# Optimization experiments

Hardware: AMD Instinct MI355X
Metric: run time of the kernel (lower is better)

The kernel has to match this reference:

```python
import jax, jax.numpy as jnp
import numpy as np
import math

D_MODEL = 256
N_LEVELS = 4
N_HEADS = 8
N_POINTS = 4
N_FRAME = 4
SHAPES = [(80, 80), (40, 40), (20, 20), (10, 10)]  # sum H*W = 8500
NB = 2
T1 = 4
T2 = 4
LEN_Q = 8500


def _grid_init_bias():
    # replicate torch _reset_parameters grid bias for sampling_offsets
    thetas = np.arange(N_HEADS, dtype=np.float32) * (2.0 * math.pi / N_HEADS)
    grid = np.stack([np.cos(thetas), np.sin(thetas)], -1)
    grid = grid / np.abs(grid).max(-1, keepdims=True)
    grid = np.tile(grid[:, None, None, :], (1, N_LEVELS, N_POINTS, 1))
    grid = grid * (np.arange(N_POINTS, dtype=np.float32) + 1.0)[None, None, :, None]
    return jnp.asarray(grid.reshape(-1), jnp.float32)


def setup_inputs() -> dict:
    key = jax.random.key(0)
    ks = jax.random.split(key, 8)
    Len_in = sum(h * w for h, w in SHAPES)
    query = jax.random.normal(ks[0], (NB, T1, LEN_Q, D_MODEL), jnp.float32)
    reference_points = jax.random.uniform(ks[1], (NB, T1, LEN_Q, N_LEVELS, 2), jnp.float32)
    input_flatten = jax.random.normal(ks[2], (NB, T2, Len_in, D_MODEL), jnp.float32)
    input_spatial_shapes = jnp.array(SHAPES, jnp.int32)
    starts = np.cumsum([0] + [h * w for h, w in SHAPES])[:-1]
    input_level_start_index = jnp.asarray(starts, jnp.int32)
    s = 0.01
    W_off = jax.random.normal(ks[3], (D_MODEL, N_HEADS * N_LEVELS * N_POINTS * 2), jnp.float32) * s
    b_off = _grid_init_bias()
    W_att = jax.random.normal(ks[4], (D_MODEL, N_HEADS * N_LEVELS * N_POINTS), jnp.float32) * s
    b_att = jnp.zeros((N_HEADS * N_LEVELS * N_POINTS,), jnp.float32)
    xav = 1.0 / math.sqrt(D_MODEL)
    W_val = jax.random.normal(ks[5], (D_MODEL, D_MODEL), jnp.float32) * xav
    b_val = jnp.zeros((D_MODEL,), jnp.float32)
    W_out = jax.random.normal(ks[6], (D_MODEL, D_MODEL), jnp.float32) * xav
    b_out = jnp.zeros((D_MODEL,), jnp.float32)
    return dict(query=query, reference_points=reference_points, input_flatten=input_flatten,
                input_spatial_shapes=input_spatial_shapes, input_level_start_index=input_level_start_index,
                W_off=W_off, b_off=b_off, W_att=W_att, b_att=b_att,
                W_val=W_val, b_val=b_val, W_out=W_out, b_out=b_out)


def _bilinear(v_flat, H, W, gx, gy):
    # v_flat: (B, d, H*W); gx,gy: (B, S) in [-1,1]; zeros padding, align_corners=False
    x = (gx + 1.0) * (W * 0.5) - 0.5
    y = (gy + 1.0) * (H * 0.5) - 0.5
    x0 = jnp.floor(x); y0 = jnp.floor(y)
    x1 = x0 + 1.0; y1 = y0 + 1.0
    wx1 = x - x0; wx0 = 1.0 - wx1
    wy1 = y - y0; wy0 = 1.0 - wy1

    def gather(xi, yi):
        valid = ((xi >= 0) & (xi < W) & (yi >= 0) & (yi < H)).astype(v_flat.dtype)
        xc = jnp.clip(xi, 0, W - 1).astype(jnp.int32)
        yc = jnp.clip(yi, 0, H - 1).astype(jnp.int32)
        idx = yc * W + xc  # (B, S)
        g = jnp.take_along_axis(v_flat, idx[:, None, :], axis=2)  # (B, d, S)
        return g * valid[:, None, :]

    return (gather(x0, y0) * (wx0 * wy0)[:, None, :]
            + gather(x1, y0) * (wx1 * wy0)[:, None, :]
            + gather(x0, y1) * (wx0 * wy1)[:, None, :]
            + gather(x1, y1) * (wx1 * wy1)[:, None, :])


def _core(value_t, locs, att, shapes):
    # value_t: (n, Len_in, M, d); locs: (n, Lq, M, L, P, 2); att: (n, Lq, M, L, P)
    n, Len_in, M, d = value_t.shape
    Lq, P = locs.shape[1], locs.shape[4]
    start = 0
    out = 0.0
    for l, (H, W) in enumerate(shapes):
        hw = H * W
        v = value_t[:, start:start + hw]  # (n, hw, M, d)
        start += hw
        v = v.transpose(0, 2, 3, 1).reshape(n * M, d, hw)
        g = locs[:, :, :, l] * 2.0 - 1.0  # (n, Lq, M, P, 2)
        g = g.transpose(0, 2, 1, 3, 4).reshape(n * M, Lq * P, 2)
        samp = _bilinear(v, H, W, g[..., 0], g[..., 1])  # (n*M, d, Lq*P)
        a = att[:, :, :, l].transpose(0, 2, 1, 3).reshape(n * M, 1, Lq * P)
        out = out + (samp * a).reshape(n, M, d, Lq, P).sum(-1)
    return out.transpose(0, 3, 1, 2).reshape(n, Lq, M * d)  # (n, Lq, C)


def reference(query, reference_points, input_flatten, input_spatial_shapes, input_level_start_index,
              W_off, b_off, W_att, b_att, W_val, b_val, W_out, b_out):
    shapes = [(int(h), int(w)) for h, w in np.asarray(input_spatial_shapes)]
    n, t1n, Lq, C = query.shape
    M, L, P = N_HEADS, N_LEVELS, N_POINTS
    d = C // M
    value = input_flatten @ W_val + b_val  # (n, T2, Len_in, C)
    value = value.reshape(n, value.shape[1], -1, M, d)
    normalizer = jnp.array([[w, h] for h, w in shapes], jnp.float32)  # (L, 2) = (W_l, H_l)
    outs = []
    for t1 in range(t1n):
        t2s = [t for t in (t1 - 1, t1, t1 + 1) if 0 <= t < N_FRAME]
        K = len(t2s)
        q = query[:, t1]  # (n, Lq, C)
        # all frames share ONE attention_weights Linear -> identical logits per t2
        logits = (q @ W_att + b_att).reshape(n, Lq, M, L, P)
        stacked = jnp.broadcast_to(logits[..., None], (n, Lq, M, L, P, K))
        att = jax.nn.softmax(stacked.reshape(n, Lq, M, L * P * K), axis=-1)
        att = att.reshape(n, Lq, M, L, P, K)
        # all frames share ONE sampling_offsets Linear -> identical locations per t2
        off = (q @ W_off + b_off).reshape(n, Lq, M, L, P, 2)
        off = off / normalizer[None, None, None, :, None, :]
        locs = reference_points[:, t1][:, :, None, :, None, :] + off  # (n,Lq,M,L,P,2)
        out_t1 = 0.0
        for k, t2 in enumerate(t2s):
            out_t1 = out_t1 + _core(value[:, t2], locs, att[..., k], shapes)
        outs.append(out_t1)
    out = jnp.stack(outs, axis=1)  # (n, T1, Lq, C)
    return out @ W_out + b_out
```

## Files before the change

### kernel.cpp

```cpp
#include <hip/hip_runtime.h>

#define LQ 8500

typedef _Float16 half8 __attribute__((ext_vector_type(8)));
typedef float f32x4 __attribute__((ext_vector_type(4)));

__device__ __forceinline__ unsigned short f2h(float f) {
    return __builtin_bit_cast(unsigned short, (_Float16)f);
}
__device__ __forceinline__ float hlo(unsigned w) {
    return (float)__builtin_bit_cast(_Float16, (unsigned short)(w & 0xffffu));
}
__device__ __forceinline__ float hhi(unsigned w) {
    return (float)__builtin_bit_cast(_Float16, (unsigned short)(w >> 16));
}
__device__ __forceinline__ unsigned pk2(float a, float b) {
    return (unsigned)f2h(a) | ((unsigned)f2h(b) << 16);
}

__global__ __launch_bounds__(256) void prep_weights(const float* __restrict__ Woff,
                                                    const float* __restrict__ boff,
                                                    const float* __restrict__ Watt,
                                                    const float* __restrict__ batt,
                                                    const float* __restrict__ Wval,
                                                    const float* __restrict__ Wout,
                                                    unsigned short* __restrict__ Wct,
                                                    unsigned short* __restrict__ Wvt,
                                                    unsigned short* __restrict__ Wot,
                                                    float* __restrict__ bcat) {
    int idx = blockIdx.x * 256 + threadIdx.x;
    if (idx < 98304) {
        int j = idx >> 8, k = idx & 255;
        float v = (j < 256) ? Woff[k * 256 + j] : Watt[k * 128 + (j - 256)];
        Wct[idx] = f2h(v);
    } else if (idx < 98304 + 65536) {
        int t = idx - 98304;
        int n = t >> 8, k = t & 255;
        Wvt[t] = f2h(Wval[k * 256 + n]);
    } else if (idx < 98304 + 131072) {
        int t = idx - 98304 - 65536;
        int n = t >> 8, k = t & 255;
        Wot[t] = f2h(Wout[k * 256 + n]);
    } else if (idx < 98304 + 131072 + 384) {
        int j = idx - 98304 - 131072;
        bcat[j] = (j < 256) ? boff[j] : batt[j - 256];
    }
}

template <int OUTMODE, int ASRC>
__global__ __launch_bounds__(256) void gemm_f16(const void* __restrict__ Avoid,
                                                const unsigned short* __restrict__ Bt,
                                                const float* __restrict__ bias,
                                                void* __restrict__ Cout, int M) {
    __shared__ char lds[32768];
    const int tid = threadIdx.x;
    const int r0 = blockIdx.x * 128, c0 = blockIdx.y * 128;
    const int wid = tid >> 6, lane = tid & 63;
    const int wr = (wid >> 1) * 64, wc = (wid & 1) * 64;

    f32x4 acc[4][4] = {};
    uint4 ra[2], rb[2];

#define LOADT(k0)                                                                      \
    {                                                                                  \
        _Pragma("unroll")                                                              \
        for (int cc = 0; cc < 2; ++cc) {                                               \
            int ch = cc * 256 + tid;                                                   \
            int row = ch >> 2, seg = ch & 3;                                           \
            uint4 va = {0, 0, 0, 0};                                                   \
            int ar = r0 + row;                                                         \
            if (ar < M) {                                                              \
                if (ASRC == 0) {                                                       \
                    va = *reinterpret_cast<const uint4*>(                              \
                        (const unsigned short*)Avoid + (size_t)ar * 256 + (k0) + seg * 8); \
                } else {                                                               \
                    const float4* ap = reinterpret_cast<const float4*>(                \
                        (const float*)Avoid + (size_t)ar * 256 + (k0) + seg * 8);      \
                    float4 a = ap[0], b = ap[1];                                       \
                    va.x = pk2(a.x, a.y); va.y = pk2(a.z, a.w);                        \
                    va.z = pk2(b.x, b.y); va.w = pk2(b.z, b.w);                        \
                }                                                                      \
            }                                                                          \
            ra[cc] = va;                                                               \
            rb[cc] = *reinterpret_cast<const uint4*>(Bt + (size_t)(c0 + row) * 256 +   \
                                                     (k0) + seg * 8);                  \
        }                                                                              \
    }

#define STORET(b)                                                                      \
    {                                                                                  \
        _Pragma("unroll")                                                              \
        for (int cc = 0; cc < 2; ++cc) {                                               \
            int ch = cc * 256 + tid;                                                   \
            int row = ch >> 2, seg = ch & 3;                                           \
            int byte = (row << 6) + (seg << 4);                                        \
            int swz = byte ^ ((row & 7) << 4);                                         \
            *reinterpret_cast<uint4*>(lds + (b) * 16384 + swz) = ra[cc];               \
            *reinterpret_cast<uint4*>(lds + (b) * 16384 + 8192 + swz) = rb[cc];        \
        }                                                                              \
    }

    LOADT(0);
    STORET(0);
    __syncthreads();

    for (int t = 0; t < 8; ++t) {
        if (t < 7) LOADT((t + 1) * 32);
        char* base = lds + (t & 1) * 16384;
        half8 af[4], bf[4];
#pragma unroll
        for (int i = 0; i < 4; ++i) {
            int rowA = wr + i * 16 + (lane & 15);
            int byteA = (rowA << 6) + ((lane >> 4) << 4);
            af[i] = *reinterpret_cast<const half8*>(base + (byteA ^ ((rowA & 7) << 4)));
            int rowB = wc + i * 16 + (lane & 15);
            int byteB = (rowB << 6) + ((lane >> 4) << 4);
            bf[i] = *reinterpret_cast<const half8*>(base + 8192 + (byteB ^ ((rowB & 7) << 4)));
        }
#pragma unroll
        for (int i = 0; i < 4; ++i)
#pragma unroll
            for (int j = 0; j < 4; ++j)
                acc[i][j] = __builtin_amdgcn_mfma_f32_16x16x32_f16(af[i], bf[j], acc[i][j], 0, 0, 0);
        if (t < 7) STORET((t + 1) & 1);
        __syncthreads();
    }

#pragma unroll
    for (int j = 0; j < 4; ++j) {
        int col = c0 + wc + j * 16 + (lane & 15);
        float bv = (OUTMODE == 3) ? 0.f : bias[col];
#pragma unroll
        for (int i = 0; i < 4; ++i) {
#pragma unroll
            for (int r = 0; r < 4; ++r) {
                int row = r0 + wr + i * 16 + (lane >> 4) * 4 + r;
                if (row >= M) continue;
                float v = acc[i][j][r];
                if (OUTMODE == 2) {
                    ((unsigned short*)Cout)[(size_t)row * 384 + col] = f2h(v + bv);
                } else if (OUTMODE == 3) {
                    ((unsigned short*)Cout)[(size_t)row * 256 + col] = f2h(v);
                } else {
                    ((float*)Cout)[(size_t)row * 256 + col] = v + bv;
                }
            }
        }
    }
#undef LOADT
#undef STORET
}

__global__ __launch_bounds__(256) void vsum_kernel(const unsigned short* __restrict__ Y,
                                                   const float* __restrict__ bval,
                                                   unsigned short* __restrict__ Vs) {
    int plane = blockIdx.y;
    int g = plane >> 3, m = plane & 7;
    int t1 = g & 3, n = g >> 2;
    int f = blockIdx.x * 256 + threadIdx.x;
    if (f >= LQ * 4) return;
    int pos = f >> 2, c8 = (f & 3) * 8;
    float Kc = (t1 == 0 || t1 == 3) ? 2.f : 3.f;
    const float* bp = bval + m * 32 + c8;
    float acc[8];
#pragma unroll
    for (int j = 0; j < 8; ++j) acc[j] = Kc * bp[j];
    int t2a = t1 == 0 ? 0 : t1 - 1;
    int t2b = t1 == 3 ? 3 : t1 + 1;
    for (int t2 = t2a; t2 <= t2b; ++t2) {
        uint4 v = *reinterpret_cast<const uint4*>(
            Y + ((size_t)(n * 4 + t2) * LQ + pos) * 256 + m * 32 + c8);
        acc[0] += hlo(v.x); acc[1] += hhi(v.x);
        acc[2] += hlo(v.y); acc[3] += hhi(v.y);
        acc[4] += hlo(v.z); acc[5] += hhi(v.z);
        acc[6] += hlo(v.w); acc[7] += hhi(v.w);
    }
    uint4 o;
    o.x = pk2(acc[0], acc[1]); o.y = pk2(acc[2], acc[3]);
    o.z = pk2(acc[4], acc[5]); o.w = pk2(acc[6], acc[7]);
    *reinterpret_cast<uint4*>(Vs + ((size_t)plane * LQ + pos) * 32 + c8) = o;
}

__global__ __launch_bounds__(256) void sample_kernel(const unsigned short* __restrict__ P,
                                                     const float* __restrict__ refp,
                                                     const unsigned short* __restrict__ Vs,
                                                     unsigned short* __restrict__ O16) {
    int tid = threadIdx.x, bid = blockIdx.x;
    int g = bid & 7;
    int q0 = (bid >> 3) * 16;
    int ql = tid >> 4, m = (tid >> 1) & 7, h = tid & 1;
    int q = q0 + ql;
    if (q >= LQ) return;

    const size_t qrow = (size_t)g * LQ + q;

    unsigned ow[16];
    {
        const uint4* po = reinterpret_cast<const uint4*>(P + qrow * 384 + m * 32);
        uint4 a = po[0], b = po[1], c = po[2], d = po[3];
        ow[0] = a.x; ow[1] = a.y; ow[2] = a.z; ow[3] = a.w;
        ow[4] = b.x; ow[5] = b.y; ow[6] = b.z; ow[7] = b.w;
        ow[8] = c.x; ow[9] = c.y; ow[10] = c.z; ow[11] = c.w;
        ow[12] = d.x; ow[13] = d.y; ow[14] = d.z; ow[15] = d.w;
    }
    float wgt[16];
    {
        const uint4* pa = reinterpret_cast<const uint4*>(P + qrow * 384 + 256 + m * 16);
        uint4 a = pa[0], b = pa[1];
        unsigned aw[8] = {a.x, a.y, a.z, a.w, b.x, b.y, b.z, b.w};
#pragma unroll
        for (int j = 0; j < 8; ++j) {
            wgt[j * 2 + 0] = hlo(aw[j]);
            wgt[j * 2 + 1] = hhi(aw[j]);
        }
        float mx = -1e30f;
#pragma unroll
        for (int j = 0; j < 16; ++j) mx = fmaxf(mx, wgt[j]);
        float s = 0.f;
#pragma unroll
        for (int j = 0; j < 16; ++j) { wgt[j] = __expf(wgt[j] - mx); s += wgt[j]; }
        int t1 = g & 3;
        float Kc = (t1 == 0 || t1 == 3) ? 2.f : 3.f;
        float inv = 1.f / (s * Kc);
#pragma unroll
        for (int j = 0; j < 16; ++j) wgt[j] *= inv;
    }

    float rx[4], ry[4];
    {
        const float4* rp = reinterpret_cast<const float4*>(refp + qrow * 8);
        float4 r0 = rp[0], r1 = rp[1];
        rx[0] = r0.x; ry[0] = r0.y; rx[1] = r0.z; ry[1] = r0.w;
        rx[2] = r1.x; ry[2] = r1.y; rx[3] = r1.z; ry[3] = r1.w;
    }

    float acc[16];
#pragma unroll
    for (int d = 0; d < 16; ++d) acc[d] = 0.f;

    const unsigned short* vplane = Vs + (size_t)(g * 8 + m) * (LQ * 32) + h * 16;

#pragma unroll 4
    for (int p = 0; p < 16; ++p) {
        const int l = p >> 2;
        const int Wl = 80 >> l;
        const int start = (l == 0) ? 0 : (l == 1) ? 6400 : (l == 2) ? 8000 : 8400;
        const float Wlf = (float)Wl;

        float x = fmaf(rx[l], Wlf, hlo(ow[p])) - 0.5f;
        float y = fmaf(ry[l], Wlf, hhi(ow[p])) - 0.5f;
        float w = wgt[p];

        float xf = floorf(x), yf = floorf(y);
        int x0 = (int)xf, y0 = (int)yf;
        float wx1 = x - xf, wy1 = y - yf;

        int xb = min(max(x0, 0), Wl - 2);
        float wl = (x0 == xb) ? 1.f - wx1 : ((x0 + 1 == xb) ? wx1 : 0.f);
        float wr = (x0 == xb) ? wx1 : ((x0 - 1 == xb) ? 1.f - wx1 : 0.f);

        int yc0 = min(max(y0, 0), Wl - 1);
        float cw0 = (y0 >= 0 && y0 < Wl) ? (1.f - wy1) * w : 0.f;
        int y1i = y0 + 1;
        int yc1 = min(max(y1i, 0), Wl - 1);
        float cw1 = (y1i >= 0 && y1i < Wl) ? wy1 * w : 0.f;

        const uint4* p0 = reinterpret_cast<const uint4*>(
            vplane + (size_t)(start + yc0 * Wl + xb) * 32);
        const uint4* p1 = reinterpret_cast<const uint4*>(
            vplane + (size_t)(start + yc1 * Wl + xb) * 32);
        uint4 L0a = p0[0], L0b = p0[1], R0a = p0[4], R0b = p0[5];
        uint4 L1a = p1[0], L1b = p1[1], R1a = p1[4], R1b = p1[5];

        float c0l = cw0 * wl, c0r = cw0 * wr;
        float c1l = cw1 * wl, c1r = cw1 * wr;

        acc[0]  += c0l * hlo(L0a.x) + c0r * hlo(R0a.x) + c1l * hlo(L1a.x) + c1r * hlo(R1a.x);
        acc[1]  += c0l * hhi(L0a.x) + c0r * hhi(R0a.x) + c1l * hhi(L1a.x) + c1r * hhi(R1a.x);
        acc[2]  += c0l * hlo(L0a.y) + c0r * hlo(R0a.y) + c1l * hlo(L1a.y) + c1r * hlo(R1a.y);
        acc[3]  += c0l * hhi(L0a.y) + c0r * hhi(R0a.y) + c1l * hhi(L1a.y) + c1r * hhi(R1a.y);
        acc[4]  += c0l * hlo(L0a.z) + c0r * hlo(R0a.z) + c1l * hlo(L1a.z) + c1r * hlo(R1a.z);
        acc[5]  += c0l * hhi(L0a.z) + c0r * hhi(R0a.z) + c1l * hhi(L1a.z) + c1r * hhi(R1a.z);
        acc[6]  += c0l * hlo(L0a.w) + c0r * hlo(R0a.w) + c1l * hlo(L1a.w) + c1r * hlo(R1a.w);
        acc[7]  += c0l * hhi(L0a.w) + c0r * hhi(R0a.w) + c1l * hhi(L1a.w) + c1r * hhi(R1a.w);
        acc[8]  += c0l * hlo(L0b.x) + c0r * hlo(R0b.x) + c1l * hlo(L1b.x) + c1r * hlo(R1b.x);
        acc[9]  += c0l * hhi(L0b.x) + c0r * hhi(R0b.x) + c1l * hhi(L1b.x) + c1r * hhi(R1b.x);
        acc[10] += c0l * hlo(L0b.y) + c0r * hlo(R0b.y) + c1l * hlo(L1b.y) + c1r * hlo(R1b.y);
        acc[11] += c0l * hhi(L0b.y) + c0r * hhi(R0b.y) + c1l * hhi(L1b.y) + c1r * hhi(R1b.y);
        acc[12] += c0l * hlo(L0b.z) + c0r * hlo(R0b.z) + c1l * hlo(L1b.z) + c1r * hlo(R1b.z);
        acc[13] += c0l * hhi(L0b.z) + c0r * hhi(R0b.z) + c1l * hhi(L1b.z) + c1r * hhi(R1b.z);
        acc[14] += c0l * hlo(L0b.w) + c0r * hlo(R0b.w) + c1l * hlo(L1b.w) + c1r * hlo(R1b.w);
        acc[15] += c0l * hhi(L0b.w) + c0r * hhi(R0b.w) + c1l * hhi(L1b.w) + c1r * hhi(R1b.w);
    }

    unsigned short* op = O16 + qrow * 256 + m * 32 + h * 16;
    uint4 o0, o1;
    o0.x = pk2(acc[0], acc[1]);   o0.y = pk2(acc[2], acc[3]);
    o0.z = pk2(acc[4], acc[5]);   o0.w = pk2(acc[6], acc[7]);
    o1.x = pk2(acc[8], acc[9]);   o1.y = pk2(acc[10], acc[11]);
    o1.z = pk2(acc[12], acc[13]); o1.w = pk2(acc[14], acc[15]);
    reinterpret_cast<uint4*>(op)[0] = o0;
    reinterpret_cast<uint4*>(op)[1] = o1;
}

extern "C" void kernel_launch(void* const* d_in, const int* in_sizes, int n_in,
                              void* d_out, int out_size, void* d_ws, size_t ws_size,
                              hipStream_t stream) {
    const float* query = (const float*)d_in[0];
    const float* refp  = (const float*)d_in[1];
    const float* inp   = (const float*)d_in[2];
    const float* Woff = (const float*)d_in[5];
    const float* boff = (const float*)d_in[6];
    const float* Watt = (const float*)d_in[7];
    const float* batt = (const float*)d_in[8];
    const float* Wval = (const float*)d_in[9];
    const float* bval = (const float*)d_in[10];
    const float* Wout = (const float*)d_in[11];
    const float* bout = (const float*)d_in[12];
    float* out = (float*)d_out;

    char* base = (char*)d_ws;
    unsigned short* Y    = (unsigned short*)base;
    unsigned short* O16  = (unsigned short*)base;
    unsigned short* Vs   = (unsigned short*)(base + 34816000);
    unsigned short* P    = (unsigned short*)(base + 69632000);
    unsigned short* Wct  = (unsigned short*)(base + 121856000);
    unsigned short* Wvt  = (unsigned short*)(base + 122052608);
    unsigned short* Wot  = (unsigned short*)(base + 122183680);
    float* bcat          = (float*)(base + 122314752);

    const int RT = (8 * LQ + 127) / 128;

    prep_weights<<<dim3(898), 256, 0, stream>>>(Woff, boff, Watt, batt, Wval, Wout,
                                                Wct, Wvt, Wot, bcat);

    gemm_f16<3, 1><<<dim3(RT, 2), 256, 0, stream>>>(inp, Wvt, bcat, Y, 8 * LQ);

    vsum_kernel<<<dim3((LQ * 4 + 255) / 256, 64), 256, 0, stream>>>(Y, bval, Vs);

    gemm_f16<2, 1><<<dim3(RT, 3), 256, 0, stream>>>(query, Wct, bcat, P, 8 * LQ);

    sample_kernel<<<dim3(((LQ + 15) / 16) * 8), 256, 0, stream>>>(P, refp, Vs, O16);

    gemm_f16<0, 0><<<dim3(RT, 2), 256, 0, stream>>>(O16, Wot, bout, out, 8 * LQ);
}
```

Measured before the change: 331.1 us.

## Merge value and query projection GEMMs and stage operands via direct global-to-LDS loads

The value projection and the query offset/attention projection are now issued as one launch with five column-block groups, so the two independent GEMMs share a grid and one launch is removed. Operand tiles that are already fp16 (weights, and both operands of the output GEMM) are copied straight into LDS with global_load_lds instead of passing through registers. An inverse-swizzle mapping keeps the existing bank-conflict-free LDS layout. The risk is correctness of the inverse swizzle against the per-wave LDS base layout, and that the output GEMM skips A rows past M, which leaves stale LDS data for those rows.

```diff
diff --git a/kernel.cpp b/kernel.cpp
--- a/kernel.cpp
+++ b/kernel.cpp
@@ -16,6 +16,12 @@
 }
 __device__ __forceinline__ unsigned pk2(float a, float b) {
     return (unsigned)f2h(a) | ((unsigned)f2h(b) << 16);
+}
+
+__device__ __forceinline__ void gl_lds16(const unsigned short* gsrc, char* ldst) {
+    __builtin_amdgcn_global_load_lds(
+        (const __attribute__((address_space(1))) void*)gsrc,
+        (__attribute__((address_space(3))) void*)ldst, 16, 0, 0);
 }
 
 __global__ __launch_bounds__(256) void prep_weights(const float* __restrict__ Woff,
@@ -47,67 +53,94 @@
     }
 }
 
-template <int OUTMODE, int ASRC>
-__global__ __launch_bounds__(256) void gemm_f16(const void* __restrict__ Avoid,
-                                                const unsigned short* __restrict__ Bt,
-                                                const float* __restrict__ bias,
-                                                void* __restrict__ Cout, int M) {
+__device__ __forceinline__ void inv_swz(int d, int& brow, int& bseg) {
+    int b8 = (d >> 8) & 1;
+    int rm = (((d >> 6) & 1) ^ b8) | (((d >> 7) & 1) << 1) | (b8 << 2);
+    int b = d ^ (rm << 4);
+    brow = b >> 6;
+    bseg = (b >> 4) & 3;
+}
+
+__global__ __launch_bounds__(256) void gemm_yp(const float* __restrict__ inp,
+                                               const float* __restrict__ query,
+                                               const unsigned short* __restrict__ Wvt,
+                                               const unsigned short* __restrict__ Wct,
+                                               const float* __restrict__ bcat,
+                                               unsigned short* __restrict__ Yo,
+                                               unsigned short* __restrict__ Po) {
     __shared__ char lds[32768];
     const int tid = threadIdx.x;
-    const int r0 = blockIdx.x * 128, c0 = blockIdx.y * 128;
+    const int r0 = blockIdx.x * 128;
+    const int yb = blockIdx.y;
+    const bool isY = yb < 2;
+    const int c0 = isY ? yb * 128 : (yb - 2) * 128;
+    const float* A = isY ? inp : query;
+    const unsigned short* Bt = isY ? Wvt : Wct;
     const int wid = tid >> 6, lane = tid & 63;
     const int wr = (wid >> 1) * 64, wc = (wid & 1) * 64;
+    const int M = 8 * LQ;
+
+    int browc[2], bsegc[2];
+#pragma unroll
+    for (int cc = 0; cc < 2; ++cc)
+        inv_swz((cc * 256 + tid) << 4, browc[cc], bsegc[cc]);
 
     f32x4 acc[4][4] = {};
-    uint4 ra[2], rb[2];
-
-#define LOADT(k0)                                                                      \
-    {                                                                                  \
-        _Pragma("unroll")                                                              \
-        for (int cc = 0; cc < 2; ++cc) {                                               \
-            int ch = cc * 256 + tid;                                                   \
-            int row = ch >> 2, seg = ch & 3;                                           \
-            uint4 va = {0, 0, 0, 0};                                                   \
-            int ar = r0 + row;                                                         \
-            if (ar < M) {                                                              \
-                if (ASRC == 0) {                                                       \
-                    va = *reinterpret_cast<const uint4*>(                              \
-                        (const unsigned short*)Avoid + (size_t)ar * 256 + (k0) + seg * 8); \
-                } else {                                                               \
-                    const float4* ap = reinterpret_cast<const float4*>(                \
-                        (const float*)Avoid + (size_t)ar * 256 + (k0) + seg * 8);      \
-                    float4 a = ap[0], b = ap[1];                                       \
-                    va.x = pk2(a.x, a.y); va.y = pk2(a.z, a.w);                        \
-                    va.z = pk2(b.x, b.y); va.w = pk2(b.z, b.w);                        \
-                }                                                                      \
-            }                                                                          \
-            ra[cc] = va;                                                               \
-            rb[cc] = *reinterpret_cast<const uint4*>(Bt + (size_t)(c0 + row) * 256 +   \
-                                                     (k0) + seg * 8);                  \
-        }                                                                              \
-    }
-
-#define STORET(b)                                                                      \
-    {                                                                                  \
-        _Pragma("unroll")                                                              \
-        for (int cc = 0; cc < 2; ++cc) {                                               \
-            int ch = cc * 256 + tid;                                                   \
-            int row = ch >> 2, seg = ch & 3;                                           \
-            int byte = (row << 6) + (seg << 4);                                        \
-            int swz = byte ^ ((row & 7) << 4);                                         \
-            *reinterpret_cast<uint4*>(lds + (b) * 16384 + swz) = ra[cc];               \
-            *reinterpret_cast<uint4*>(lds + (b) * 16384 + 8192 + swz) = rb[cc];        \
-        }                                                                              \
-    }
-
-    LOADT(0);
-    STORET(0);
+    uint4 ra[2];
+
+#define LOADA(k0)                                                                   \
+    {                                                                               \
+        _Pragma("unroll")                                                           \
+        for (int cc = 0; cc < 2; ++cc) {                                            \
+            int ch = cc * 256 + tid;                                               \
+            int row = ch >> 2, seg = ch & 3;                                        \
+            uint4 va = {0, 0, 0, 0};                                               \
+            int ar = r0 + row;                                                      \
+            if (ar < M) {                                                           \
+                const float4* ap = reinterpret_cast<const float4*>(                 \
+                    A + (size_t)ar * 256 + (k0) + seg * 8);                         \
+                float4 a = ap[0], b = ap[1];                                        \
+                va.x = pk2(a.x, a.y); va.y = pk2(a.z, a.w);                         \
+                va.z = pk2(b.x, b.y); va.w = pk2(b.z, b.w);                         \
+            }                                                                       \
+            ra[cc] = va;                                                            \
+        }                                                                           \
+    }
+
+#define STOREA(bf)                                                                  \
+    {                                                                               \
+        _Pragma("unroll")                                                           \
+        for (int cc = 0; cc < 2; ++cc) {                                            \
+            int ch = cc * 256 + tid;                                               \
+            int row = ch >> 2, seg = ch & 3;                                        \
+            int byte = (row << 6) + (seg << 4);                                     \
+            int swzb = byte ^ ((row & 7) << 4);                                     \
+            *reinterpret_cast<uint4*>(lds + (bf) * 16384 + swzb) = ra[cc];          \
+        }                                                                           \
+    }
+
+#define LOADB(bf, k0)                                                               \
+    {                                                                               \
+        _Pragma("unroll")                                                           \
+        for (int cc = 0; cc < 2; ++cc) {                                            \
+            const unsigned short* gs =                                              \
+                Bt + (size_t)(c0 + browc[cc]) * 256 + (k0) + bsegc[cc] * 8;         \
+            gl_lds16(gs, lds + (bf) * 16384 + 8192 + cc * 4096 + wid * 1024);       \
+        }                                                                           \
+    }
+
+    LOADA(0);
+    LOADB(0, 0);
+    STOREA(0);
     __syncthreads();
 
     for (int t = 0; t < 8; ++t) {
-        if (t < 7) LOADT((t + 1) * 32);
+        if (t < 7) {
+            LOADB((t + 1) & 1, (t + 1) * 32);
+            LOADA((t + 1) * 32);
+        }
         char* base = lds + (t & 1) * 16384;
-        half8 af[4], bf[4];
+        half8 af[4], bfr[4];
 #pragma unroll
         for (int i = 0; i < 4; ++i) {
             int rowA = wr + i * 16 + (lane & 15);
@@ -115,40 +148,108 @@
             af[i] = *reinterpret_cast<const half8*>(base + (byteA ^ ((rowA & 7) << 4)));
             int rowB = wc + i * 16 + (lane & 15);
             int byteB = (rowB << 6) + ((lane >> 4) << 4);
-            bf[i] = *reinterpret_cast<const half8*>(base + 8192 + (byteB ^ ((rowB & 7) << 4)));
+            bfr[i] = *reinterpret_cast<const half8*>(base + 8192 + (byteB ^ ((rowB & 7) << 4)));
         }
 #pragma unroll
         for (int i = 0; i < 4; ++i)
 #pragma unroll
             for (int j = 0; j < 4; ++j)
-                acc[i][j] = __builtin_amdgcn_mfma_f32_16x16x32_f16(af[i], bf[j], acc[i][j], 0, 0, 0);
-        if (t < 7) STORET((t + 1) & 1);
+                acc[i][j] = __builtin_amdgcn_mfma_f32_16x16x32_f16(af[i], bfr[j], acc[i][j], 0, 0, 0);
+        if (t < 7) STOREA((t + 1) & 1);
         __syncthreads();
     }
 
 #pragma unroll
     for (int j = 0; j < 4; ++j) {
         int col = c0 + wc + j * 16 + (lane & 15);
-        float bv = (OUTMODE == 3) ? 0.f : bias[col];
+        float bv = isY ? 0.f : bcat[col];
 #pragma unroll
         for (int i = 0; i < 4; ++i) {
 #pragma unroll
             for (int r = 0; r < 4; ++r) {
                 int row = r0 + wr + i * 16 + (lane >> 4) * 4 + r;
                 if (row >= M) continue;
-                float v = acc[i][j][r];
-                if (OUTMODE == 2) {
-                    ((unsigned short*)Cout)[(size_t)row * 384 + col] = f2h(v + bv);
-                } else if (OUTMODE == 3) {
-                    ((unsigned short*)Cout)[(size_t)row * 256 + col] = f2h(v);
-                } else {
-                    ((float*)Cout)[(size_t)row * 256 + col] = v + bv;
-                }
+                float v = acc[i][j][r] + bv;
+                if (isY) Yo[(size_t)row * 256 + col] = f2h(v);
+                else     Po[(size_t)row * 384 + col] = f2h(v);
             }
         }
     }
-#undef LOADT
-#undef STORET
+#undef LOADA
+#undef STOREA
+#undef LOADB
+}
+
+__global__ __launch_bounds__(256) void gemm_out(const unsigned short* __restrict__ O16,
+                                                const unsigned short* __restrict__ Wot,
+                                                const float* __restrict__ bout,
+                                                float* __restrict__ out) {
+    __shared__ char lds[32768];
+    const int tid = threadIdx.x;
+    const int r0 = blockIdx.x * 128, c0 = blockIdx.y * 128;
+    const int wid = tid >> 6, lane = tid & 63;
+    const int wr = (wid >> 1) * 64, wc = (wid & 1) * 64;
+    const int M = 8 * LQ;
+
+    int browc[2], bsegc[2];
+#pragma unroll
+    for (int cc = 0; cc < 2; ++cc)
+        inv_swz((cc * 256 + tid) << 4, browc[cc], bsegc[cc]);
+
+    f32x4 acc[4][4] = {};
+
+#define STAGE(bf, k0)                                                               \
+    {                                                                               \
+        _Pragma("unroll")                                                           \
+        for (int cc = 0; cc < 2; ++cc) {                                            \
+            char* lbase = lds + (bf) * 16384 + cc * 4096 + wid * 1024;              \
+            int ar = r0 + browc[cc];                                                \
+            if (ar < M)                                                             \
+                gl_lds16(O16 + (size_t)ar * 256 + (k0) + bsegc[cc] * 8, lbase);     \
+            gl_lds16(Wot + (size_t)(c0 + browc[cc]) * 256 + (k0) + bsegc[cc] * 8,   \
+                     lbase + 8192);                                                 \
+        }                                                                           \
+    }
+
+    STAGE(0, 0);
+    __syncthreads();
+
+    for (int t = 0; t < 8; ++t) {
+        if (t < 7) STAGE((t + 1) & 1, (t + 1) * 32);
+        char* base = lds + (t & 1) * 16384;
+        half8 af[4], bfr[4];
+#pragma unroll
+        for (int i = 0; i < 4; ++i) {
+            int rowA = wr + i * 16 + (lane & 15);
+            int byteA = (rowA << 6) + ((lane >> 4) << 4);
+            af[i] = *reinterpret_cast<const half8*>(base + (byteA ^ ((rowA & 7) << 4)));
+            int rowB = wc + i * 16 + (lane & 15);
+            int byteB = (rowB << 6) + ((lane >> 4) << 4);
+            bfr[i] = *reinterpret_cast<const half8*>(base + 8192 + (byteB ^ ((rowB & 7) << 4)));
+        }
+#pragma unroll
+        for (int i = 0; i < 4; ++i)
+#pragma unroll
+            for (int j = 0; j < 4; ++j)
+                acc[i][j] = __builtin_amdgcn_mfma_f32_16x16x32_f16(af[i], bfr[j], acc[i][j], 0, 0, 0);
+        __syncthreads();
+    }
+
+#pragma unroll
+    for (int j = 0; j < 4; ++j) {
+        int col = c0 + wc + j * 16 + (lane & 15);
+        float bv = bout[col];
+#pragma unroll
+        for (int i = 0; i < 4; ++i) {
+#pragma unroll
+            for (int r = 0; r < 4; ++r) {
+                int row = r0 + wr + i * 16 + (lane >> 4) * 4 + r;
+                if (row >= M) continue;
+                out[(size_t)row * 256 + col] = acc[i][j][r] + bv;
+            }
+        }
+    }
+#undef STAGE
 }
 
 __global__ __launch_bounds__(256) void vsum_kernel(const unsigned short* __restrict__ Y,
@@ -334,13 +435,11 @@
     prep_weights<<<dim3(898), 256, 0, stream>>>(Woff, boff, Watt, batt, Wval, Wout,
                                                 Wct, Wvt, Wot, bcat);
 
-    gemm_f16<3, 1><<<dim3(RT, 2), 256, 0, stream>>>(inp, Wvt, bcat, Y, 8 * LQ);
+    gemm_yp<<<dim3(RT, 5), 256, 0, stream>>>(inp, query, Wvt, Wct, bcat, Y, P);
 
     vsum_kernel<<<dim3((LQ * 4 + 255) / 256, 64), 256, 0, stream>>>(Y, bval, Vs);
 
-    gemm_f16<2, 1><<<dim3(RT, 3), 256, 0, stream>>>(query, Wct, bcat, P, 8 * LQ);
-
     sample_kernel<<<dim3(((LQ + 15) / 16) * 8), 256, 0, stream>>>(P, refp, Vs, O16);
 
-    gemm_f16<0, 0><<<dim3(RT, 2), 256, 0, stream>>>(O16, Wot, bout, out, 8 * LQ);
-}
+    gemm_out<<<dim3(RT, 2), 256, 0, stream>>>(O16, Wot, bout, out);
+}
```

After: 310.0 us, median of 2. -6.4%, faster.
